# Performance work log

Measured on AMD Instinct MI355X. Metric: run time of the kernel, lower is better.

The kernel has to match this reference:

```python
import jax, jax.numpy as jnp
import numpy as np

F_DIM = 128
RBF_DIM = 20
N_NODES = 10000
N_EDGES = 200000
CUTOFF = 5


def setup_inputs() -> dict:
    key = jax.random.key(0)
    ks = jax.random.split(key, 12)
    s = jax.random.normal(ks[0], (N_NODES, F_DIM), jnp.float32)
    vec = jax.random.normal(ks[1], (N_NODES, 3, F_DIM), jnp.float32)
    edge_indexes = jax.random.randint(ks[2], (2, N_EDGES), 0, N_NODES, jnp.int32)
    edge_vector = jax.random.normal(ks[3], (N_EDGES, 3), jnp.float32)
    # distances in (0.5, 5.0) so fcut is nontrivial and no divide-by-zero
    edge_distance = jax.random.uniform(ks[4], (N_EDGES,), jnp.float32) * 4.5 + 0.5
    edge_rbf = jax.random.normal(ks[5], (N_EDGES, RBF_DIM), jnp.float32)
    # params: linear_s = Linear(F,F) -> SiLU -> Linear(F,3F); linear_rbf = Linear(RBF,3F)
    Ws1 = jax.random.normal(ks[6], (F_DIM, F_DIM), jnp.float32) / np.sqrt(F_DIM)
    bs1 = jnp.zeros((F_DIM,), jnp.float32)
    Ws2 = jax.random.normal(ks[7], (3 * F_DIM, F_DIM), jnp.float32) / np.sqrt(F_DIM)
    bs2 = jnp.zeros((3 * F_DIM,), jnp.float32)
    Wrbf = jax.random.normal(ks[8], (3 * F_DIM, RBF_DIM), jnp.float32) / np.sqrt(RBF_DIM)
    brbf = jnp.zeros((3 * F_DIM,), jnp.float32)
    return {
        "s": s, "vec": vec, "edge_vector": edge_vector,
        "edge_distance": edge_distance, "edge_rbf": edge_rbf,
        "Ws1": Ws1, "bs1": bs1, "Ws2": Ws2, "bs2": bs2,
        "Wrbf": Wrbf, "brbf": brbf,
        "edge_indexes": edge_indexes, "cutoff_dist": CUTOFF,
    }


def reference(s, vec, edge_vector, edge_distance, edge_rbf,
              Ws1, bs1, Ws2, bs2, Wrbf, brbf,
              edge_indexes, cutoff_dist):
    num_atoms, nf = s.shape
    dst_recv = edge_indexes[0]   # index_add target (message receivers)
    src_send = edge_indexes[1]   # gather source (message senders)

    S = s[src_send]              # [E, F]
    Vec = vec[src_send]          # [E, 3, F]

    # linear_s: Linear -> SiLU -> Linear
    h = jax.nn.silu(S @ Ws1.T + bs1)          # [E, F]
    phi = h @ Ws2.T + bs2                      # [E, 3F]

    rbf_lin = edge_rbf @ Wrbf.T + brbf         # [E, 3F]
    # cosine cutoff: 0.5*(cos(pi*d/rc)+1) for d < rc else 0
    rc = jnp.asarray(cutoff_dist, edge_distance.dtype)
    fcut = 0.5 * (jnp.cos(jnp.pi * edge_distance / rc) + 1.0)
    fcut = jnp.where(edge_distance < rc, fcut, 0.0)

    W = rbf_lin * fcut[:, None]
    vec_Ws, vec_Wvv, vec_Wvs = jnp.split(phi * W, 3, axis=-1)  # each [E, F]

    ds = jnp.zeros((num_atoms, nf), s.dtype).at[dst_recv].add(vec_Ws)

    vec_n = edge_vector / edge_distance[:, None]               # [E, 3]
    dVec = vec_Wvv[:, None, :] * Vec + vec_n[:, :, None] * vec_Wvs[:, None, :]  # [E,3,F]
    dvec = jnp.zeros((num_atoms, 3, nf), s.dtype).at[dst_recv].add(dVec)

    return ds, dvec
```

## Files before the change

kernel.cpp:

```cpp
#include <hip/hip_runtime.h>
#include <hip/hip_bf16.h>

typedef __attribute__((ext_vector_type(8))) short short8;
typedef __attribute__((ext_vector_type(4))) float floatx4;
typedef _Float16 half2_t __attribute__((ext_vector_type(2)));

#define CAP 64

__device__ __forceinline__ unsigned short f2bf(float x) {
    unsigned u = __float_as_uint(x);
    unsigned r = u + 0x7fffu + ((u >> 16) & 1u);
    return (unsigned short)(r >> 16);
}
__device__ __forceinline__ float bf2f(unsigned short h) {
    return __uint_as_float(((unsigned)h) << 16);
}
__device__ __forceinline__ unsigned short f2h(float x) {
    _Float16 h = (_Float16)x;
    return __builtin_bit_cast(unsigned short, h);
}
__device__ __forceinline__ float FD(unsigned int a, unsigned int b, float c) {
#if __has_builtin(__builtin_amdgcn_fdot2)
    return __builtin_amdgcn_fdot2(__builtin_bit_cast(half2_t, a),
                                  __builtin_bit_cast(half2_t, b), c, false);
#else
    half2_t ha = __builtin_bit_cast(half2_t, a);
    half2_t hb = __builtin_bit_cast(half2_t, b);
    return c + (float)ha[0] * (float)hb[0] + (float)ha[1] * (float)hb[1];
#endif
}
__device__ __forceinline__ float decode_rc(const void* cutoff_raw) {
    float fv = ((const float*)cutoff_raw)[0];
    int   iv = ((const int*)cutoff_raw)[0];
    if (fv > 0.099f && fv < 1.0e6f) return fv;
    if (iv > 0 && iv < 1000000) return (float)iv;
    double dv = ((const double*)cutoff_raw)[0];
    if (dv > 0.099 && dv < 1.0e6) return (float)dv;
    return (float)(((const long long*)cutoff_raw)[0]);
}

__global__ void setup_kernel(const float* __restrict__ vec,
                             const float* __restrict__ Ws1,
                             const float* __restrict__ Ws2,
                             const float* __restrict__ Wrbf,
                             const float* __restrict__ edge_rbf,
                             const int* __restrict__ eidx,
                             const float* __restrict__ edge_vec,
                             const float* __restrict__ edge_dist,
                             const void* __restrict__ cutoff_raw,
                             unsigned short* __restrict__ P6,
                             unsigned short* __restrict__ ws1_bf,
                             unsigned short* __restrict__ ws2_bf,
                             unsigned short* __restrict__ wrbf_h,
                             unsigned short* __restrict__ rbf_h,
                             int* __restrict__ cnt,
                             unsigned int* __restrict__ rec,
                             int ng_vec, int ng_w1, int ng_w2, int ng_wh, int ng_rh,
                             int RB, int E, int nbc)
{
    int tid = threadIdx.x;
    if ((int)blockIdx.x < nbc) {
        int total = ng_vec + ng_w1 + ng_w2 + ng_wh + ng_rh;
        int stride = nbc * 256;
        for (int g = blockIdx.x * 256 + tid; g < total; g += stride) {
            if (g < ng_vec) {
                int node = g / 48;
                int r = (g - node * 48) * 8;
                const float4* sp = (const float4*)(vec + (size_t)node * 384 + r);
                float4 x0 = sp[0], x1 = sp[1];
                short8 v;
                v[0]=(short)f2bf(x0.x); v[1]=(short)f2bf(x0.y);
                v[2]=(short)f2bf(x0.z); v[3]=(short)f2bf(x0.w);
                v[4]=(short)f2bf(x1.x); v[5]=(short)f2bf(x1.y);
                v[6]=(short)f2bf(x1.z); v[7]=(short)f2bf(x1.w);
                *(short8*)(P6 + (size_t)node * 768 + 384 + r) = v;
            } else if (g < ng_vec + ng_w1 + ng_w2) {
                int j = (g - ng_vec) * 8;
                const float* srcp;
                unsigned short* dstp;
                if (j < ng_w1 * 8) { srcp = Ws1 + j; dstp = ws1_bf + j; }
                else               { srcp = Ws2 + (j - ng_w1 * 8); dstp = ws2_bf + (j - ng_w1 * 8); }
                float4 x0 = ((const float4*)srcp)[0], x1 = ((const float4*)srcp)[1];
                short8 v;
                v[0]=(short)f2bf(x0.x); v[1]=(short)f2bf(x0.y);
                v[2]=(short)f2bf(x0.z); v[3]=(short)f2bf(x0.w);
                v[4]=(short)f2bf(x1.x); v[5]=(short)f2bf(x1.y);
                v[6]=(short)f2bf(x1.z); v[7]=(short)f2bf(x1.w);
                *(short8*)dstp = v;
            } else if (g < ng_vec + ng_w1 + ng_w2 + ng_wh) {
                int gg = g - ng_vec - ng_w1 - ng_w2;
                int n = gg >> 2, k0 = (gg & 3) * 8;
                short8 v;
                #pragma unroll
                for (int t = 0; t < 8; ++t) {
                    int k = k0 + t;
                    v[t] = (k < RB) ? (short)f2h(Wrbf[(size_t)n * RB + k]) : (short)0;
                }
                *(short8*)(wrbf_h + n * 32 + k0) = v;
            } else {
                int gg = g - ng_vec - ng_w1 - ng_w2 - ng_wh;
                int e = gg / 3, k0 = (gg - e * 3) * 8;
                short8 v;
                #pragma unroll
                for (int t = 0; t < 8; ++t) {
                    int k = k0 + t;
                    v[t] = (k < RB) ? (short)f2h(edge_rbf[(size_t)e * RB + k]) : (short)0;
                }
                *(short8*)(rbf_h + (size_t)e * 24 + k0) = v;
            }
        }
    } else {
        int i = ((int)blockIdx.x - nbc) * 256 + tid;
        if (i >= E) return;
        float rc = decode_rc(cutoff_raw);
        int d = eidx[i];
        int slot = atomicAdd(&cnt[d], 1);
        if (slot >= CAP) return;
        float dist = edge_dist[i];
        float fc = 0.0f;
        if (dist < rc) fc = 0.5f * (cosf(3.14159265358979323846f * dist / rc) + 1.0f);
        float inv = 1.0f / dist;
        unsigned int* rp = rec + ((size_t)(d * CAP + slot) << 3);
        ((uint4*)rp)[0] = make_uint4((unsigned)eidx[E + i], (unsigned)i, 0u, 0u);
        ((uint4*)rp)[1] = make_uint4(__float_as_uint(edge_vec[i * 3 + 0] * inv),
                                     __float_as_uint(edge_vec[i * 3 + 1] * inv),
                                     __float_as_uint(edge_vec[i * 3 + 2] * inv),
                                     __float_as_uint(fc));
    }
}

#define LN 136
__global__ __launch_bounds__(256, 4)
void node_kernel(const float* __restrict__ s,
                 const unsigned short* __restrict__ ws1_bf,
                 const float* __restrict__ bs1,
                 const unsigned short* __restrict__ ws2_bf,
                 const float* __restrict__ bs2,
                 unsigned short* __restrict__ P6,
                 int Nn)
{
    const int tid  = threadIdx.x;
    const int wv   = tid >> 6;
    const int lane = tid & 63;
    const int l15  = lane & 15;
    const int qq   = lane >> 4;
    const int base = blockIdx.x * 16;

    __shared__ unsigned short S_bf[16][LN];
    __shared__ unsigned short H_bf[16][LN];

    {
        int row = tid >> 4;
        int col = (tid & 15) * 8;
        int node = base + row;
        short8 v;
        if (node < Nn) {
            const float4* sp4 = (const float4*)(s + (size_t)node * 128 + col);
            float4 x0 = sp4[0], x1 = sp4[1];
            v[0] = (short)f2bf(x0.x); v[1] = (short)f2bf(x0.y);
            v[2] = (short)f2bf(x0.z); v[3] = (short)f2bf(x0.w);
            v[4] = (short)f2bf(x1.x); v[5] = (short)f2bf(x1.y);
            v[6] = (short)f2bf(x1.z); v[7] = (short)f2bf(x1.w);
        } else {
            #pragma unroll
            for (int k = 0; k < 8; ++k) v[k] = 0;
        }
        *((short8*)&S_bf[row][col]) = v;
    }
    __syncthreads();

    {
        short8 a[4];
        #pragma unroll
        for (int ks = 0; ks < 4; ++ks)
            a[ks] = *((const short8*)&S_bf[l15][ks * 32 + qq * 8]);
        floatx4 acc1[2];
        #pragma unroll
        for (int t = 0; t < 2; ++t) acc1[t] = (floatx4){0.f, 0.f, 0.f, 0.f};
        #pragma unroll
        for (int ks = 0; ks < 4; ++ks) {
            #pragma unroll
            for (int t = 0; t < 2; ++t) {
                int nj = wv * 2 + t;
                short8 b = *((const short8*)(ws1_bf + ((nj * 16 + l15) * 128 + ks * 32 + qq * 8)));
                acc1[t] = __builtin_amdgcn_mfma_f32_16x16x32_bf16(a[ks], b, acc1[t], 0, 0, 0);
            }
        }
        #pragma unroll
        for (int t = 0; t < 2; ++t) {
            int nj = wv * 2 + t;
            float b1 = bs1[nj * 16 + l15];
            #pragma unroll
            for (int r = 0; r < 4; ++r) {
                float x = acc1[t][r] + b1;
                float h = x / (1.0f + __expf(-x));
                H_bf[qq * 4 + r][nj * 16 + l15] = f2bf(h);
            }
        }
    }
    __syncthreads();

    {
        short8 a[4];
        #pragma unroll
        for (int ks = 0; ks < 4; ++ks)
            a[ks] = *((const short8*)&H_bf[l15][ks * 32 + qq * 8]);
        #pragma unroll
        for (int t6 = 0; t6 < 6; ++t6) {
            int t = wv * 6 + t6;
            int n = t * 16 + l15;
            floatx4 acc = (floatx4){0.f, 0.f, 0.f, 0.f};
            #pragma unroll
            for (int ks = 0; ks < 4; ++ks) {
                short8 b = *((const short8*)(ws2_bf + ((size_t)n * 128 + ks * 32 + qq * 8)));
                acc = __builtin_amdgcn_mfma_f32_16x16x32_bf16(a[ks], b, acc, 0, 0, 0);
            }
            float b2 = bs2[n];
            #pragma unroll
            for (int r = 0; r < 4; ++r) {
                int node = base + qq * 4 + r;
                if (node < Nn)
                    P6[(size_t)node * 768 + n] = f2bf(acc[r] + b2);
            }
        }
    }
}

__global__ __launch_bounds__(256, 6)
void edge_kernel(const unsigned short* __restrict__ P6,
                 const unsigned short* __restrict__ wrbf_h,
                 const float* __restrict__ brbf,
                 const int* __restrict__ cnt,
                 const unsigned int* __restrict__ rec,
                 const unsigned short* __restrict__ rbf_h,
                 float* __restrict__ out_ds,
                 float* __restrict__ out_dvec,
                 int Nn)
{
    const int tid  = threadIdx.x;
    const int w    = tid >> 6;
    const int lane = tid & 63;
    const int node = __builtin_amdgcn_readfirstlane((int)blockIdx.x * 2 + (w >> 1));
    const int c    = (w & 1) * 64 + lane;
    if (node >= Nn) return;

    const unsigned short* wp0 = wrbf_h + ((size_t)c << 5);
    const unsigned short* wp1 = wrbf_h + ((size_t)(128 + c) << 5);
    const unsigned short* wp2 = wrbf_h + ((size_t)(256 + c) << 5);
    uint4 w0a = *(const uint4*)wp0;
    uint4 w0b = *(const uint4*)(wp0 + 8);
    uint2 w0c = *(const uint2*)(wp0 + 16);
    uint4 w1a = *(const uint4*)wp1;
    uint4 w1b = *(const uint4*)(wp1 + 8);
    uint2 w1c = *(const uint2*)(wp1 + 16);
    uint4 w2a = *(const uint4*)wp2;
    uint4 w2b = *(const uint4*)(wp2 + 8);
    uint2 w2c = *(const uint2*)(wp2 + 16);
    float b0 = brbf[c];
    float b1 = brbf[128 + c];
    float b2 = brbf[256 + c];
    asm volatile("" : "+v"(w0a.x), "+v"(w0a.y), "+v"(w0a.z), "+v"(w0a.w),
                      "+v"(w0b.x), "+v"(w0b.y), "+v"(w0b.z), "+v"(w0b.w),
                      "+v"(w0c.x), "+v"(w0c.y));
    asm volatile("" : "+v"(w1a.x), "+v"(w1a.y), "+v"(w1a.z), "+v"(w1a.w),
                      "+v"(w1b.x), "+v"(w1b.y), "+v"(w1b.z), "+v"(w1b.w),
                      "+v"(w1c.x), "+v"(w1c.y));
    asm volatile("" : "+v"(w2a.x), "+v"(w2a.y), "+v"(w2a.z), "+v"(w2a.w),
                      "+v"(w2b.x), "+v"(w2b.y), "+v"(w2b.z), "+v"(w2b.w),
                      "+v"(w2c.x), "+v"(w2c.y),
                      "+v"(b0), "+v"(b1), "+v"(b2));

    const int deg = min(cnt[node], CAP);
    const size_t bb = (size_t)node * CAP;

    float as = 0.f, a0 = 0.f, a1 = 0.f, a2 = 0.f;

    if (deg > 0) {
        const uint4* rp = (const uint4*)(rec + (bb << 3));
        uint4 sm = rp[0], mq = rp[1];
        const unsigned short* rr = rbf_h + (size_t)(int)sm.y * 24;
        uint4 Ra = *(const uint4*)rr;
        uint4 Rb = *(const uint4*)(rr + 8);
        uint2 Rc = *(const uint2*)(rr + 16);

        for (int sl = 0; sl < deg; ++sl) {
            const unsigned short* pr = P6 + (size_t)(int)sm.x * 768;
            unsigned short u0 = pr[c];
            unsigned short u1 = pr[128 + c];
            unsigned short u2 = pr[256 + c];
            unsigned short u3 = pr[384 + c];
            unsigned short u4 = pr[512 + c];
            unsigned short u5 = pr[640 + c];

            int np = (sl + 1 < deg) ? (sl + 1) : sl;
            uint4 smn = rp[2 * np], mqn = rp[2 * np + 1];
            const unsigned short* rrn = rbf_h + (size_t)(int)smn.y * 24;
            uint4 Ran = *(const uint4*)rrn;
            uint4 Rbn = *(const uint4*)(rrn + 8);
            uint2 Rcn = *(const uint2*)(rrn + 16);

            float d0 = b0, d1 = b1, d2 = b2;
            d0 = FD(Ra.x, w0a.x, d0); d1 = FD(Ra.x, w1a.x, d1); d2 = FD(Ra.x, w2a.x, d2);
            d0 = FD(Ra.y, w0a.y, d0); d1 = FD(Ra.y, w1a.y, d1); d2 = FD(Ra.y, w2a.y, d2);
            d0 = FD(Ra.z, w0a.z, d0); d1 = FD(Ra.z, w1a.z, d1); d2 = FD(Ra.z, w2a.z, d2);
            d0 = FD(Ra.w, w0a.w, d0); d1 = FD(Ra.w, w1a.w, d1); d2 = FD(Ra.w, w2a.w, d2);
            d0 = FD(Rb.x, w0b.x, d0); d1 = FD(Rb.x, w1b.x, d1); d2 = FD(Rb.x, w2b.x, d2);
            d0 = FD(Rb.y, w0b.y, d0); d1 = FD(Rb.y, w1b.y, d1); d2 = FD(Rb.y, w2b.y, d2);
            d0 = FD(Rb.z, w0b.z, d0); d1 = FD(Rb.z, w1b.z, d1); d2 = FD(Rb.z, w2b.z, d2);
            d0 = FD(Rb.w, w0b.w, d0); d1 = FD(Rb.w, w1b.w, d1); d2 = FD(Rb.w, w2b.w, d2);
            d0 = FD(Rc.x, w0c.x, d0); d1 = FD(Rc.x, w1c.x, d1); d2 = FD(Rc.x, w2c.x, d2);
            d0 = FD(Rc.y, w0c.y, d0); d1 = FD(Rc.y, w1c.y, d1); d2 = FD(Rc.y, w2c.y, d2);

            float ps = bf2f(u0), pv = bf2f(u1), px = bf2f(u2);
            float v0 = bf2f(u3), v1 = bf2f(u4), v2 = bf2f(u5);

            float fc = __uint_as_float(mq.w);
            float W0 = d0 * fc, W1 = d1 * fc, W2 = d2 * fc;
            as = fmaf(ps, W0, as);
            float mv = pv * W1;
            float mx = px * W2;
            a0 = fmaf(mv, v0, fmaf(mx, __uint_as_float(mq.x), a0));
            a1 = fmaf(mv, v1, fmaf(mx, __uint_as_float(mq.y), a1));
            a2 = fmaf(mv, v2, fmaf(mx, __uint_as_float(mq.z), a2));

            sm = smn; mq = mqn; Ra = Ran; Rb = Rbn; Rc = Rcn;
        }
    }

    __builtin_nontemporal_store(as, out_ds + (size_t)node * 128 + c);
    float* od = out_dvec + (size_t)node * 384;
    __builtin_nontemporal_store(a0, od + c);
    __builtin_nontemporal_store(a1, od + 128 + c);
    __builtin_nontemporal_store(a2, od + 256 + c);
}

extern "C" void kernel_launch(void* const* d_in, const int* in_sizes, int n_in,
                              void* d_out, int out_size, void* d_ws, size_t ws_size,
                              hipStream_t stream) {
    const float* s        = (const float*)d_in[0];
    const float* vec      = (const float*)d_in[1];
    const float* edge_vec = (const float*)d_in[2];
    const float* edge_dst = (const float*)d_in[3];
    const float* edge_rbf = (const float*)d_in[4];
    const float* Ws1      = (const float*)d_in[5];
    const float* bs1      = (const float*)d_in[6];
    const float* Ws2      = (const float*)d_in[7];
    const float* bs2      = (const float*)d_in[8];
    const float* Wrbf     = (const float*)d_in[9];
    const float* brbf     = (const float*)d_in[10];
    const int*   eidx     = (const int*)d_in[11];
    const void*  cutoff   = d_in[12];

    const int F  = 128;
    const int Nn = in_sizes[0] / F;
    const int E  = in_sizes[3];
    const int RB = in_sizes[4] / E;
    const int F3 = 3 * F;

    unsigned int*   rec     = (unsigned int*)d_ws;
    unsigned short* P6      = (unsigned short*)(rec + (size_t)Nn * CAP * 8);
    unsigned short* rbf_h   = P6 + (size_t)Nn * 768;
    unsigned short* ws1_bf  = rbf_h + (size_t)E * 24;
    unsigned short* ws2_bf  = ws1_bf + F * F;
    unsigned short* wrbf_h  = ws2_bf + (size_t)F3 * F;
    int* cnt                = (int*)(wrbf_h + F3 * 32);

    int ng_vec = (Nn * F3) >> 3;
    int ng_w1  = (F * F) >> 3;
    int ng_w2  = (F3 * F) >> 3;
    int ng_wh  = (F3 * 32) >> 3;
    int ng_rh  = (E * 24) >> 3;

    hipMemsetAsync(cnt, 0, (size_t)Nn * sizeof(int), stream);

    {
        long long total = (long long)ng_vec + ng_w1 + ng_w2 + ng_wh + ng_rh;
        int nbc = (int)((total + 255) / 256);
        int nbb = (E + 255) / 256;
        setup_kernel<<<nbc + nbb, 256, 0, stream>>>(vec, Ws1, Ws2, Wrbf, edge_rbf,
                                                    eidx, edge_vec, edge_dst, cutoff,
                                                    P6, ws1_bf, ws2_bf, wrbf_h, rbf_h,
                                                    cnt, rec,
                                                    ng_vec, ng_w1, ng_w2, ng_wh, ng_rh,
                                                    RB, E, nbc);
    }
    node_kernel<<<(Nn + 15) / 16, 256, 0, stream>>>(s, ws1_bf, bs1, ws2_bf, bs2, P6, Nn);

    float* out_ds   = (float*)d_out;
    float* out_dvec = out_ds + (size_t)Nn * F;

    edge_kernel<<<(Nn + 1) / 2, 256, 0, stream>>>(P6, wrbf_h, brbf,
                                                  cnt, rec, rbf_h,
                                                  out_ds, out_dvec, Nn);
}
```

Baseline: 203.3 us.

## Merge node MLP, edge bucketing and casts into one produce kernel

Fuses setup_kernel and node_kernel into a single launch whose blocks are split by role: node MLP blocks, edge-bucketing blocks, and cast blocks. The node MLP now converts Ws1/Ws2 from fp32 to bf16 on the fly instead of reading pre-converted copies, which removes the weight-cast pass and its workspace. This saves one launch and the serial dependency between setup and node stages. In exchange, every node block re-reads fp32 weights and repeats the conversion, and the fused kernel carries shared memory and a 4-wave occupancy bound even for the cast and bucketing roles.

```diff
diff --git a/kernel.cpp b/kernel.cpp
--- a/kernel.cpp
+++ b/kernel.cpp
@@ -18,6 +18,14 @@
 __device__ __forceinline__ unsigned short f2h(float x) {
     _Float16 h = (_Float16)x;
     return __builtin_bit_cast(unsigned short, h);
+}
+__device__ __forceinline__ short8 cvt8(float4 x0, float4 x1) {
+    short8 v;
+    v[0] = (short)f2bf(x0.x); v[1] = (short)f2bf(x0.y);
+    v[2] = (short)f2bf(x0.z); v[3] = (short)f2bf(x0.w);
+    v[4] = (short)f2bf(x1.x); v[5] = (short)f2bf(x1.y);
+    v[6] = (short)f2bf(x1.z); v[7] = (short)f2bf(x1.w);
+    return v;
 }
 __device__ __forceinline__ float FD(unsigned int a, unsigned int b, float c) {
 #if __has_builtin(__builtin_amdgcn_fdot2)
@@ -39,78 +47,117 @@
     return (float)(((const long long*)cutoff_raw)[0]);
 }
 
-__global__ void setup_kernel(const float* __restrict__ vec,
-                             const float* __restrict__ Ws1,
-                             const float* __restrict__ Ws2,
-                             const float* __restrict__ Wrbf,
-                             const float* __restrict__ edge_rbf,
-                             const int* __restrict__ eidx,
-                             const float* __restrict__ edge_vec,
-                             const float* __restrict__ edge_dist,
-                             const void* __restrict__ cutoff_raw,
-                             unsigned short* __restrict__ P6,
-                             unsigned short* __restrict__ ws1_bf,
-                             unsigned short* __restrict__ ws2_bf,
-                             unsigned short* __restrict__ wrbf_h,
-                             unsigned short* __restrict__ rbf_h,
-                             int* __restrict__ cnt,
-                             unsigned int* __restrict__ rec,
-                             int ng_vec, int ng_w1, int ng_w2, int ng_wh, int ng_rh,
-                             int RB, int E, int nbc)
+#define LN 136
+__global__ __launch_bounds__(256, 4)
+void produce_kernel(const float* __restrict__ s,
+                    const float* __restrict__ vec,
+                    const float* __restrict__ Ws1,
+                    const float* __restrict__ bs1,
+                    const float* __restrict__ Ws2,
+                    const float* __restrict__ bs2,
+                    const float* __restrict__ Wrbf,
+                    const float* __restrict__ edge_rbf,
+                    const int* __restrict__ eidx,
+                    const float* __restrict__ edge_vec,
+                    const float* __restrict__ edge_dist,
+                    const void* __restrict__ cutoff_raw,
+                    unsigned short* __restrict__ P6,
+                    unsigned short* __restrict__ wrbf_h,
+                    unsigned short* __restrict__ rbf_h,
+                    int* __restrict__ cnt,
+                    unsigned int* __restrict__ rec,
+                    int Nn, int RB, int E,
+                    int nb_node, int nb_sc,
+                    int ng_vec, int ng_wh, int ng_rh)
 {
-    int tid = threadIdx.x;
-    if ((int)blockIdx.x < nbc) {
-        int total = ng_vec + ng_w1 + ng_w2 + ng_wh + ng_rh;
-        int stride = nbc * 256;
-        for (int g = blockIdx.x * 256 + tid; g < total; g += stride) {
-            if (g < ng_vec) {
-                int node = g / 48;
-                int r = (g - node * 48) * 8;
-                const float4* sp = (const float4*)(vec + (size_t)node * 384 + r);
-                float4 x0 = sp[0], x1 = sp[1];
-                short8 v;
-                v[0]=(short)f2bf(x0.x); v[1]=(short)f2bf(x0.y);
-                v[2]=(short)f2bf(x0.z); v[3]=(short)f2bf(x0.w);
-                v[4]=(short)f2bf(x1.x); v[5]=(short)f2bf(x1.y);
-                v[6]=(short)f2bf(x1.z); v[7]=(short)f2bf(x1.w);
-                *(short8*)(P6 + (size_t)node * 768 + 384 + r) = v;
-            } else if (g < ng_vec + ng_w1 + ng_w2) {
-                int j = (g - ng_vec) * 8;
-                const float* srcp;
-                unsigned short* dstp;
-                if (j < ng_w1 * 8) { srcp = Ws1 + j; dstp = ws1_bf + j; }
-                else               { srcp = Ws2 + (j - ng_w1 * 8); dstp = ws2_bf + (j - ng_w1 * 8); }
-                float4 x0 = ((const float4*)srcp)[0], x1 = ((const float4*)srcp)[1];
-                short8 v;
-                v[0]=(short)f2bf(x0.x); v[1]=(short)f2bf(x0.y);
-                v[2]=(short)f2bf(x0.z); v[3]=(short)f2bf(x0.w);
-                v[4]=(short)f2bf(x1.x); v[5]=(short)f2bf(x1.y);
-                v[6]=(short)f2bf(x1.z); v[7]=(short)f2bf(x1.w);
-                *(short8*)dstp = v;
-            } else if (g < ng_vec + ng_w1 + ng_w2 + ng_wh) {
-                int gg = g - ng_vec - ng_w1 - ng_w2;
-                int n = gg >> 2, k0 = (gg & 3) * 8;
-                short8 v;
-                #pragma unroll
-                for (int t = 0; t < 8; ++t) {
-                    int k = k0 + t;
-                    v[t] = (k < RB) ? (short)f2h(Wrbf[(size_t)n * RB + k]) : (short)0;
-                }
-                *(short8*)(wrbf_h + n * 32 + k0) = v;
+    const int bid = (int)blockIdx.x;
+    const int tid = threadIdx.x;
+
+    __shared__ unsigned short S_bf[16][LN];
+    __shared__ unsigned short H_bf[16][LN];
+
+    if (bid < nb_node) {
+        const int wv   = tid >> 6;
+        const int lane = tid & 63;
+        const int l15  = lane & 15;
+        const int qq   = lane >> 4;
+        const int base = bid * 16;
+
+        {
+            int row = tid >> 4;
+            int col = (tid & 15) * 8;
+            int node = base + row;
+            short8 v;
+            if (node < Nn) {
+                const float4* sp4 = (const float4*)(s + (size_t)node * 128 + col);
+                v = cvt8(sp4[0], sp4[1]);
             } else {
-                int gg = g - ng_vec - ng_w1 - ng_w2 - ng_wh;
-                int e = gg / 3, k0 = (gg - e * 3) * 8;
-                short8 v;
-                #pragma unroll
-                for (int t = 0; t < 8; ++t) {
-                    int k = k0 + t;
-                    v[t] = (k < RB) ? (short)f2h(edge_rbf[(size_t)e * RB + k]) : (short)0;
-                }
-                *(short8*)(rbf_h + (size_t)e * 24 + k0) = v;
-            }
-        }
-    } else {
-        int i = ((int)blockIdx.x - nbc) * 256 + tid;
+                #pragma unroll
+                for (int k = 0; k < 8; ++k) v[k] = 0;
+            }
+            *((short8*)&S_bf[row][col]) = v;
+        }
+        __syncthreads();
+
+        {
+            short8 a[4];
+            #pragma unroll
+            for (int ks = 0; ks < 4; ++ks)
+                a[ks] = *((const short8*)&S_bf[l15][ks * 32 + qq * 8]);
+            floatx4 acc1[2];
+            #pragma unroll
+            for (int t = 0; t < 2; ++t) acc1[t] = (floatx4){0.f, 0.f, 0.f, 0.f};
+            #pragma unroll
+            for (int ks = 0; ks < 4; ++ks) {
+                #pragma unroll
+                for (int t = 0; t < 2; ++t) {
+                    int nj = wv * 2 + t;
+                    const float* wr = Ws1 + (size_t)(nj * 16 + l15) * 128 + ks * 32 + qq * 8;
+                    short8 b = cvt8(((const float4*)wr)[0], ((const float4*)wr)[1]);
+                    acc1[t] = __builtin_amdgcn_mfma_f32_16x16x32_bf16(a[ks], b, acc1[t], 0, 0, 0);
+                }
+            }
+            #pragma unroll
+            for (int t = 0; t < 2; ++t) {
+                int nj = wv * 2 + t;
+                float b1 = bs1[nj * 16 + l15];
+                #pragma unroll
+                for (int r = 0; r < 4; ++r) {
+                    float x = acc1[t][r] + b1;
+                    float h = x / (1.0f + __expf(-x));
+                    H_bf[qq * 4 + r][nj * 16 + l15] = f2bf(h);
+                }
+            }
+        }
+        __syncthreads();
+
+        {
+            short8 a[4];
+            #pragma unroll
+            for (int ks = 0; ks < 4; ++ks)
+                a[ks] = *((const short8*)&H_bf[l15][ks * 32 + qq * 8]);
+            #pragma unroll
+            for (int t6 = 0; t6 < 6; ++t6) {
+                int t = wv * 6 + t6;
+                int n = t * 16 + l15;
+                floatx4 acc = (floatx4){0.f, 0.f, 0.f, 0.f};
+                #pragma unroll
+                for (int ks = 0; ks < 4; ++ks) {
+                    const float* wr = Ws2 + (size_t)n * 128 + ks * 32 + qq * 8;
+                    short8 b = cvt8(((const float4*)wr)[0], ((const float4*)wr)[1]);
+                    acc = __builtin_amdgcn_mfma_f32_16x16x32_bf16(a[ks], b, acc, 0, 0, 0);
+                }
+                float b2 = bs2[n];
+                #pragma unroll
+                for (int r = 0; r < 4; ++r) {
+                    int node = base + qq * 4 + r;
+                    if (node < Nn)
+                        P6[(size_t)node * 768 + n] = f2bf(acc[r] + b2);
+                }
+            }
+        }
+    } else if (bid < nb_node + nb_sc) {
+        int i = (bid - nb_node) * 256 + tid;
         if (i >= E) return;
         float rc = decode_rc(cutoff_raw);
         int d = eidx[i];
@@ -126,101 +173,36 @@
                                      __float_as_uint(edge_vec[i * 3 + 1] * inv),
                                      __float_as_uint(edge_vec[i * 3 + 2] * inv),
                                      __float_as_uint(fc));
-    }
-}
-
-#define LN 136
-__global__ __launch_bounds__(256, 4)
-void node_kernel(const float* __restrict__ s,
-                 const unsigned short* __restrict__ ws1_bf,
-                 const float* __restrict__ bs1,
-                 const unsigned short* __restrict__ ws2_bf,
-                 const float* __restrict__ bs2,
-                 unsigned short* __restrict__ P6,
-                 int Nn)
-{
-    const int tid  = threadIdx.x;
-    const int wv   = tid >> 6;
-    const int lane = tid & 63;
-    const int l15  = lane & 15;
-    const int qq   = lane >> 4;
-    const int base = blockIdx.x * 16;
-
-    __shared__ unsigned short S_bf[16][LN];
-    __shared__ unsigned short H_bf[16][LN];
-
-    {
-        int row = tid >> 4;
-        int col = (tid & 15) * 8;
-        int node = base + row;
-        short8 v;
-        if (node < Nn) {
-            const float4* sp4 = (const float4*)(s + (size_t)node * 128 + col);
-            float4 x0 = sp4[0], x1 = sp4[1];
-            v[0] = (short)f2bf(x0.x); v[1] = (short)f2bf(x0.y);
-            v[2] = (short)f2bf(x0.z); v[3] = (short)f2bf(x0.w);
-            v[4] = (short)f2bf(x1.x); v[5] = (short)f2bf(x1.y);
-            v[6] = (short)f2bf(x1.z); v[7] = (short)f2bf(x1.w);
-        } else {
-            #pragma unroll
-            for (int k = 0; k < 8; ++k) v[k] = 0;
-        }
-        *((short8*)&S_bf[row][col]) = v;
-    }
-    __syncthreads();
-
-    {
-        short8 a[4];
-        #pragma unroll
-        for (int ks = 0; ks < 4; ++ks)
-            a[ks] = *((const short8*)&S_bf[l15][ks * 32 + qq * 8]);
-        floatx4 acc1[2];
-        #pragma unroll
-        for (int t = 0; t < 2; ++t) acc1[t] = (floatx4){0.f, 0.f, 0.f, 0.f};
-        #pragma unroll
-        for (int ks = 0; ks < 4; ++ks) {
-            #pragma unroll
-            for (int t = 0; t < 2; ++t) {
-                int nj = wv * 2 + t;
-                short8 b = *((const short8*)(ws1_bf + ((nj * 16 + l15) * 128 + ks * 32 + qq * 8)));
-                acc1[t] = __builtin_amdgcn_mfma_f32_16x16x32_bf16(a[ks], b, acc1[t], 0, 0, 0);
-            }
-        }
-        #pragma unroll
-        for (int t = 0; t < 2; ++t) {
-            int nj = wv * 2 + t;
-            float b1 = bs1[nj * 16 + l15];
-            #pragma unroll
-            for (int r = 0; r < 4; ++r) {
-                float x = acc1[t][r] + b1;
-                float h = x / (1.0f + __expf(-x));
-                H_bf[qq * 4 + r][nj * 16 + l15] = f2bf(h);
-            }
-        }
-    }
-    __syncthreads();
-
-    {
-        short8 a[4];
-        #pragma unroll
-        for (int ks = 0; ks < 4; ++ks)
-            a[ks] = *((const short8*)&H_bf[l15][ks * 32 + qq * 8]);
-        #pragma unroll
-        for (int t6 = 0; t6 < 6; ++t6) {
-            int t = wv * 6 + t6;
-            int n = t * 16 + l15;
-            floatx4 acc = (floatx4){0.f, 0.f, 0.f, 0.f};
-            #pragma unroll
-            for (int ks = 0; ks < 4; ++ks) {
-                short8 b = *((const short8*)(ws2_bf + ((size_t)n * 128 + ks * 32 + qq * 8)));
-                acc = __builtin_amdgcn_mfma_f32_16x16x32_bf16(a[ks], b, acc, 0, 0, 0);
-            }
-            float b2 = bs2[n];
-            #pragma unroll
-            for (int r = 0; r < 4; ++r) {
-                int node = base + qq * 4 + r;
-                if (node < Nn)
-                    P6[(size_t)node * 768 + n] = f2bf(acc[r] + b2);
+    } else {
+        int total = ng_vec + ng_wh + ng_rh;
+        int nbc = (int)gridDim.x - nb_node - nb_sc;
+        int stride = nbc * 256;
+        for (int g = (bid - nb_node - nb_sc) * 256 + tid; g < total; g += stride) {
+            if (g < ng_vec) {
+                int node = g / 48;
+                int r = (g - node * 48) * 8;
+                const float4* sp = (const float4*)(vec + (size_t)node * 384 + r);
+                *(short8*)(P6 + (size_t)node * 768 + 384 + r) = cvt8(sp[0], sp[1]);
+            } else if (g < ng_vec + ng_wh) {
+                int gg = g - ng_vec;
+                int n = gg >> 2, k0 = (gg & 3) * 8;
+                short8 v;
+                #pragma unroll
+                for (int t = 0; t < 8; ++t) {
+                    int k = k0 + t;
+                    v[t] = (k < RB) ? (short)f2h(Wrbf[(size_t)n * RB + k]) : (short)0;
+                }
+                *(short8*)(wrbf_h + n * 32 + k0) = v;
+            } else {
+                int gg = g - ng_vec - ng_wh;
+                int e = gg / 3, k0 = (gg - e * 3) * 8;
+                short8 v;
+                #pragma unroll
+                for (int t = 0; t < 8; ++t) {
+                    int k = k0 + t;
+                    v[t] = (k < RB) ? (short)f2h(edge_rbf[(size_t)e * RB + k]) : (short)0;
+                }
+                *(short8*)(rbf_h + (size_t)e * 24 + k0) = v;
             }
         }
     }
@@ -360,31 +342,26 @@
     unsigned int*   rec     = (unsigned int*)d_ws;
     unsigned short* P6      = (unsigned short*)(rec + (size_t)Nn * CAP * 8);
     unsigned short* rbf_h   = P6 + (size_t)Nn * 768;
-    unsigned short* ws1_bf  = rbf_h + (size_t)E * 24;
-    unsigned short* ws2_bf  = ws1_bf + F * F;
-    unsigned short* wrbf_h  = ws2_bf + (size_t)F3 * F;
+    unsigned short* wrbf_h  = rbf_h + (size_t)E * 24;
     int* cnt                = (int*)(wrbf_h + F3 * 32);
 
     int ng_vec = (Nn * F3) >> 3;
-    int ng_w1  = (F * F) >> 3;
-    int ng_w2  = (F3 * F) >> 3;
     int ng_wh  = (F3 * 32) >> 3;
     int ng_rh  = (E * 24) >> 3;
 
     hipMemsetAsync(cnt, 0, (size_t)Nn * sizeof(int), stream);
 
-    {
-        long long total = (long long)ng_vec + ng_w1 + ng_w2 + ng_wh + ng_rh;
-        int nbc = (int)((total + 255) / 256);
-        int nbb = (E + 255) / 256;
-        setup_kernel<<<nbc + nbb, 256, 0, stream>>>(vec, Ws1, Ws2, Wrbf, edge_rbf,
-                                                    eidx, edge_vec, edge_dst, cutoff,
-                                                    P6, ws1_bf, ws2_bf, wrbf_h, rbf_h,
-                                                    cnt, rec,
-                                                    ng_vec, ng_w1, ng_w2, ng_wh, ng_rh,
-                                                    RB, E, nbc);
-    }
-    node_kernel<<<(Nn + 15) / 16, 256, 0, stream>>>(s, ws1_bf, bs1, ws2_bf, bs2, P6, Nn);
+    int nb_node = (Nn + 15) / 16;
+    int nb_sc   = (E + 255) / 256;
+    long long total_g = (long long)ng_vec + ng_wh + ng_rh;
+    int nb_cast = (int)((total_g + 255) / 256);
+
+    produce_kernel<<<nb_node + nb_sc + nb_cast, 256, 0, stream>>>(
+        s, vec, Ws1, bs1, Ws2, bs2, Wrbf, edge_rbf,
+        eidx, edge_vec, edge_dst, cutoff,
+        P6, wrbf_h, rbf_h, cnt, rec,
+        Nn, RB, E, nb_node, nb_sc,
+        ng_vec, ng_wh, ng_rh);
 
     float* out_ds   = (float*)d_out;
     float* out_dvec = out_ds + (size_t)Nn * F;
```

Measured after the change: 194.5 us. 4.3% less time.
